# Kernel tuning notes

Hardware: AMD Instinct MI355X
Metric: run time of the kernel (lower is better)

The kernel has to match this reference:

```python
import jax, jax.numpy as jnp
import numpy as np

GRID_SIZE = 4
SPLINE_ORDER = 3
EDGE_DIM = 384


def make_grid():
    # efficient-KAN default grid_range [-1, 1]
    h = 2.0 / GRID_SIZE
    return (jnp.arange(-SPLINE_ORDER, GRID_SIZE + SPLINE_ORDER + 1, dtype=jnp.float32) * h - 1.0)


def b_splines(x, grid, k):
    # x: (N, d); grid: (G+2k+1,) shared across features -> (N, d, G+k)
    xe = x[..., None]
    bases = ((xe >= grid[:-1]) & (xe < grid[1:])).astype(x.dtype)
    for j in range(1, k + 1):
        bases = ((xe - grid[: -(j + 1)]) / (grid[j:-1] - grid[: -(j + 1)]) * bases[..., :-1]
                 + (grid[j + 1:] - xe) / (grid[j + 1:] - grid[1:-j]) * bases[..., 1:])
    return bases


def kan_linear(x, base_W, spline_W, grid):
    # efficient-KAN KANLinear: silu base path + spline path
    base = jax.nn.silu(x) @ base_W.T
    B = b_splines(x, grid, SPLINE_ORDER)          # (N, in, G+k)
    spline = jnp.einsum('nic,oic->no', B, spline_W)
    return base + spline


def gckan_layer(x, edge_index, edge_attr, p, grid):
    ea = edge_attr @ p['edge_W'].T + p['edge_b']          # (E, out)
    xt = x @ p['node_W'].T + p['node_b']                  # (N, out)
    row, col = edge_index[0], edge_index[1]
    msg = ea * xt[row]                                    # gather + multiply
    agg = jnp.zeros_like(xt).at[col].add(msg)             # scatter-add
    return kan_linear(agg, p['base_W'], p['spline_W'], grid)


def _layer_params(key, in_feat, out_feat):
    k1, k2, k3, k4 = jax.random.split(key, 4)
    coef = GRID_SIZE + SPLINE_ORDER
    return {
        'node_W': jax.random.normal(k1, (out_feat, in_feat), jnp.float32) / np.sqrt(in_feat),
        'node_b': jnp.zeros((out_feat,), jnp.float32),
        'edge_W': jax.random.normal(k2, (out_feat, EDGE_DIM), jnp.float32) / np.sqrt(EDGE_DIM),
        'edge_b': jnp.zeros((out_feat,), jnp.float32),
        'base_W': jax.random.normal(k3, (out_feat, out_feat), jnp.float32) / np.sqrt(out_feat),
        'spline_W': jax.random.normal(k4, (out_feat, out_feat, coef), jnp.float32) * (0.1 / np.sqrt(out_feat)),
    }


def setup_inputs() -> dict:
    N, E, F, H, C = 50000, 500000, 256, 256, 32
    key = jax.random.key(0)
    ks = jax.random.split(key, 6)
    inp = {
        'x': jax.random.normal(ks[0], (N, F), jnp.float32),
        'edge_index': jax.random.randint(ks[1], (2, E), 0, N, jnp.int32),
        'edge_attr': jax.random.normal(ks[2], (E, EDGE_DIM), jnp.float32),
    }
    p0 = _layer_params(ks[3], F, H)
    p1 = _layer_params(ks[4], H, H)
    po = _layer_params(ks[5], F + 2 * H, C)
    for tag, p in (('0', p0), ('1', p1), ('o', po)):
        for n, v in p.items():
            inp[n + tag] = v
    return inp


def reference(x, edge_index, edge_attr,
              node_W0, node_b0, edge_W0, edge_b0, base_W0, spline_W0,
              node_W1, node_b1, edge_W1, edge_b1, base_W1, spline_W1,
              node_Wo, node_bo, edge_Wo, edge_bo, base_Wo, spline_Wo):
    grid = make_grid()
    p0 = dict(node_W=node_W0, node_b=node_b0, edge_W=edge_W0, edge_b=edge_b0, base_W=base_W0, spline_W=spline_W0)
    p1 = dict(node_W=node_W1, node_b=node_b1, edge_W=edge_W1, edge_b=edge_b1, base_W=base_W1, spline_W=spline_W1)
    po = dict(node_W=node_Wo, node_b=node_bo, edge_W=edge_Wo, edge_b=edge_bo, base_W=base_Wo, spline_W=spline_Wo)
    skips = [x]
    h = gckan_layer(x, edge_index, edge_attr, p0, grid)
    skips.append(h)
    h = gckan_layer(h, edge_index, edge_attr, p1, grid)
    skips.append(h)
    h = jnp.concatenate(skips, axis=1)  # skip=True concat -> (N, F+2H)
    return gckan_layer(h, edge_index, edge_attr, po, grid)
```

## Files before the change

kernel.cpp:

```cpp
#include <hip/hip_runtime.h>


typedef __attribute__((ext_vector_type(4))) float f32x4;
typedef __attribute__((ext_vector_type(8))) short bf16x8;
typedef __attribute__((ext_vector_type(8))) unsigned short u16x8;
typedef __attribute__((ext_vector_type(4))) unsigned short u16x4;

__device__ __forceinline__ unsigned short f2bf(float f) {
    union { float f; unsigned u; } v; v.f = f;
    unsigned r = v.u + 0x7FFFu + ((v.u >> 16) & 1u);
    return (unsigned short)(r >> 16);
}

__device__ __forceinline__ float bf2f(unsigned short u) {
    union { unsigned u; float f; } v; v.u = ((unsigned)u) << 16;
    return v.f;
}

__device__ __forceinline__ float siluf(float x) {
    return x / (1.0f + __expf(-x));
}

__device__ __forceinline__ void gl16(const void* g, void* l) {
    __builtin_amdgcn_global_load_lds(
        (const __attribute__((address_space(1))) unsigned*)g,
        (__attribute__((address_space(3))) unsigned*)l, 16, 0, 0);
}

__device__ __forceinline__ void expand8(float x, float* o8) {
    float b[10];
#pragma unroll
    for (int i = 0; i < 10; ++i) {
        float ti = 0.5f * i - 2.5f;
        b[i] = (x >= ti && x < ti + 0.5f) ? 1.0f : 0.0f;
    }
#pragma unroll
    for (int j = 1; j <= 3; ++j) {
        float inv = 2.0f / (float)j;
#pragma unroll
        for (int i = 0; i < 10 - j; ++i) {
            float ti = 0.5f * i - 2.5f;
            float tj = 0.5f * (i + j + 1) - 2.5f;
            b[i] = (x - ti) * inv * b[i] + (tj - x) * inv * b[i + 1];
        }
    }
    o8[0] = siluf(x);
#pragma unroll
    for (int c = 0; c < 7; ++c) o8[c + 1] = b[c];
}

__global__ __launch_bounds__(256) void k_hist(
    const int* __restrict__ col, int* __restrict__ cnt, int E) {
    int i = blockIdx.x * 256 + threadIdx.x;
    if (i < E) atomicAdd(&cnt[col[i]], 1);
}

__global__ __launch_bounds__(1024) void k_scan(int* __restrict__ c, int N) {
    __shared__ int wsum[16];
    __shared__ int ctot;
    const int t = threadIdx.x;
    const int lane = t & 63, wid = t >> 6;
    int carry = 0;
    for (int base = 0; base < N; base += 1024) {
        int i = base + t;
        int v0 = (i < N) ? c[i] : 0;
        int v = v0;
#pragma unroll
        for (int off = 1; off < 64; off <<= 1) {
            int n = __shfl_up(v, (unsigned)off, 64);
            if (lane >= off) v += n;
        }
        if (lane == 63) wsum[wid] = v;
        __syncthreads();
        if (t < 16) {
            int s = wsum[t], sv = s;
#pragma unroll
            for (int off = 1; off < 16; off <<= 1) {
                int n = __shfl_up(sv, (unsigned)off, 16);
                if (t >= off) sv += n;
            }
            wsum[t] = sv - s;
            if (t == 15) ctot = sv;
        }
        __syncthreads();
        if (i < N) c[i] = carry + wsum[wid] + v - v0;
        carry += ctot;
        __syncthreads();
    }
}

__global__ __launch_bounds__(256) void k_scatter(
    const int* __restrict__ row, const int* __restrict__ col,
    int* __restrict__ cursor, int* __restrict__ rowS,
    int* __restrict__ colS, int* __restrict__ eidS, int E) {
    int i = blockIdx.x * 256 + threadIdx.x;
    if (i < E) {
        int c = col[i];
        int p = atomicAdd(&cursor[c], 1);
        rowS[p] = row[i];
        colS[p] = c;
        eidS[p] = i;
    }
}

__global__ __launch_bounds__(256) void pack_kt(
    const float* __restrict__ src, unsigned short* __restrict__ dst,
    int N, int K) {
    long idx = (long)blockIdx.x * 256 + threadIdx.x;
    if (idx >= (long)N * K) return;
    int n = (int)(idx / K), k = (int)(idx - (long)n * K);
    long o = (((long)(k >> 5) * 4 + ((k >> 3) & 3)) * N + n) * 8 + (k & 7);
    dst[o] = f2bf(src[idx]);
}

__global__ __launch_bounds__(256) void pack_kan_kt(
    const float* __restrict__ baseW, const float* __restrict__ splineW,
    unsigned short* __restrict__ dst, int N) {
    long idx = (long)blockIdx.x * 256 + threadIdx.x;
    if (idx >= (long)N * 2048) return;
    int n = (int)(idx >> 11), k = (int)(idx & 2047);
    int ic = k >> 3, c = k & 7;
    float v = (c == 0) ? baseW[(long)n * 256 + ic]
                       : splineW[((long)n * 256 + ic) * 7 + (c - 1)];
    long o = (((long)(k >> 5) * 4 + ((k >> 3) & 3)) * N + n) * 8 + (k & 7);
    dst[o] = f2bf(v);
}

template <bool TWO, bool WITH_O>
__global__ __launch_bounds__(256, 2) void ea_gemm7(
    const float* __restrict__ EA,
    const unsigned short* __restrict__ Wp0, const float* __restrict__ b0,
    const unsigned short* __restrict__ Wp1, const float* __restrict__ b1,
    const unsigned short* __restrict__ Wpo, const float* __restrict__ bo,
    unsigned short* __restrict__ O0, unsigned short* __restrict__ O1,
    unsigned short* __restrict__ Oo, int E) {
    constexpr int BSZ = TWO ? 32768 : 16384;
    constexpr int WOOFF = 8192 + 2 * BSZ;
    constexpr int SMEMSZ = WOOFF + (WITH_O ? 4096 : 0);
    __shared__ __align__(16) char smem[SMEMSZ];

    const int tid = threadIdx.x;
    const int wv = tid >> 6, lane = tid & 63;
    const int l15 = lane & 15, l4 = lane >> 4;
    const long m0 = (long)blockIdx.x * 64;

    f32x4 acc0[4][4] = {};
    f32x4 acc1[4][4] = {};
    f32x4 acco[4] = {};

    const int sr = tid >> 2, sg = tid & 3;
    const long arow = m0 + sr;
    const bool aok = arow < E;
    const float* aptr = EA + arow * 384 + sg * 8;
    const int awoff = sg * 1024 + ((sr ^ (sg << 2))) * 16;

    const char* wp0 = (const char*)Wp0;
    const char* wp1 = (const char*)Wp1;
    const char* wpo = (const char*)Wpo;
    const int ci = lane * 16;

#define ISSUE_B7(IT, BUF)                                                      \
    {                                                                          \
        _Pragma("unroll")                                                      \
        for (int g = 0; g < 4; ++g) {                                          \
            int ch = g * 4 + wv;                                               \
            gl16(wp0 + (long)(IT) * 16384 + ch * 1024 + ci,                    \
                 smem + 8192 + (BUF) * BSZ + ch * 1024);                       \
        }                                                                      \
        if (TWO) {                                                             \
            _Pragma("unroll")                                                  \
            for (int g = 0; g < 4; ++g) {                                      \
                int ch = g * 4 + wv;                                           \
                gl16(wp1 + (long)(IT) * 16384 + ch * 1024 + ci,                \
                     smem + 8192 + (BUF) * BSZ + 16384 + ch * 1024);           \
            }                                                                  \
        }                                                                      \
        __builtin_amdgcn_sched_barrier(0);                                     \
    }

#define ISSUE_WO7(IT, BUF)                                                     \
    {                                                                          \
        if (WITH_O && wv >= 2)                                                 \
            gl16(wpo + (long)(IT) * 2048 + (wv - 2) * 1024 + ci,               \
                 smem + WOOFF + (BUF) * 2048 + (wv - 2) * 1024);               \
        __builtin_amdgcn_sched_barrier(0);                                     \
    }

#define WRITE_A7(IT, VA, VB)                                                   \
    {                                                                          \
        u16x8 rr = {};                                                         \
        if (aok) {                                                             \
            rr[0] = f2bf((VA).x); rr[1] = f2bf((VA).y);                        \
            rr[2] = f2bf((VA).z); rr[3] = f2bf((VA).w);                        \
            rr[4] = f2bf((VB).x); rr[5] = f2bf((VB).y);                        \
            rr[6] = f2bf((VB).z); rr[7] = f2bf((VB).w);                        \
        }                                                                      \
        *(u16x8*)(smem + ((IT) & 1) * 4096 + awoff) = rr;                      \
        __builtin_amdgcn_sched_barrier(0);                                     \
    }

    const float4 z4 = make_float4(0.f, 0.f, 0.f, 0.f);
    {
        float4 s0 = z4, s1 = z4;
        if (aok) { s0 = *(const float4*)(aptr); s1 = *(const float4*)(aptr + 4); }
        WRITE_A7(0, s0, s1);
    }
    float4 r1a = z4, r1b = z4, r0a = z4, r0b = z4;
    if (aok) { r1a = *(const float4*)(aptr + 32); r1b = *(const float4*)(aptr + 36); }
    __builtin_amdgcn_sched_barrier(0);
    ISSUE_B7(0, 0);
    ISSUE_WO7(0, 0);
    if (aok) { r0a = *(const float4*)(aptr + 64); r0b = *(const float4*)(aptr + 68); }
    __builtin_amdgcn_sched_barrier(0);

#pragma unroll
    for (int it = 0; it < 12; ++it) {
        if (it <= 9) asm volatile("s_waitcnt vmcnt(2)" ::: "memory");
        else         asm volatile("s_waitcnt vmcnt(0)" ::: "memory");
        asm volatile("s_waitcnt lgkmcnt(0)" ::: "memory");
        __builtin_amdgcn_s_barrier();
        __builtin_amdgcn_sched_barrier(0);

        if (it < 11) {
            const int nbf = (it + 1) & 1;
            ISSUE_B7(it + 1, nbf);
            ISSUE_WO7(it + 1, nbf);
            if ((it + 1) & 1) { WRITE_A7(it + 1, r1a, r1b); }
            else              { WRITE_A7(it + 1, r0a, r0b); }
            if (it <= 8) {
                if ((it + 3) & 1) {
                    if (aok) {
                        r1a = *(const float4*)(aptr + (it + 3) * 32);
                        r1b = *(const float4*)(aptr + (it + 3) * 32 + 4);
                    }
                } else {
                    if (aok) {
                        r0a = *(const float4*)(aptr + (it + 3) * 32);
                        r0b = *(const float4*)(aptr + (it + 3) * 32 + 4);
                    }
                }
                __builtin_amdgcn_sched_barrier(0);
            }
        }

        const int buf = it & 1;
        bf16x8 af[4];
#pragma unroll
        for (int mi = 0; mi < 4; ++mi)
            af[mi] = *(const bf16x8*)(smem + buf * 4096 + l4 * 1024 +
                                      (((mi * 16 + l15) ^ (l4 << 2))) * 16);
        {
            bf16x8 bf0[4];
#pragma unroll
            for (int nj = 0; nj < 4; ++nj)
                bf0[nj] = *(const bf16x8*)(smem + 8192 + buf * BSZ + l4 * 4096 +
                                           (wv * 64 + nj * 16 + l15) * 16);
#pragma unroll
            for (int mi = 0; mi < 4; ++mi)
#pragma unroll
                for (int nj = 0; nj < 4; ++nj)
                    acc0[mi][nj] = __builtin_amdgcn_mfma_f32_16x16x32_bf16(
                        af[mi], bf0[nj], acc0[mi][nj], 0, 0, 0);
        }
        if (TWO) {
            bf16x8 bf1[4];
#pragma unroll
            for (int nj = 0; nj < 4; ++nj)
                bf1[nj] = *(const bf16x8*)(smem + 8192 + buf * BSZ + 16384 +
                                           l4 * 4096 + (wv * 64 + nj * 16 + l15) * 16);
#pragma unroll
            for (int mi = 0; mi < 4; ++mi)
#pragma unroll
                for (int nj = 0; nj < 4; ++nj)
                    acc1[mi][nj] = __builtin_amdgcn_mfma_f32_16x16x32_bf16(
                        af[mi], bf1[nj], acc1[mi][nj], 0, 0, 0);
        }
        if (WITH_O && wv < 2) {
            bf16x8 bov = *(const bf16x8*)(smem + WOOFF + buf * 2048 + l4 * 512 +
                                          (wv * 16 + l15) * 16);
#pragma unroll
            for (int mi = 0; mi < 4; ++mi)
                acco[mi] = __builtin_amdgcn_mfma_f32_16x16x32_bf16(
                    af[mi], bov, acco[mi], 0, 0, 0);
        }
    }
#undef ISSUE_B7
#undef ISSUE_WO7
#undef WRITE_A7

    const int nb2 = wv * 64;
    float bs0[4];
#pragma unroll
    for (int nj = 0; nj < 4; ++nj) bs0[nj] = b0[nb2 + nj * 16 + l15];
#pragma unroll
    for (int mi = 0; mi < 4; ++mi) {
#pragma unroll
        for (int r = 0; r < 4; ++r) {
            long e = m0 + mi * 16 + l4 * 4 + r;
            if (e < E) {
                unsigned short* dst = O0 + e * 256 + nb2 + l15;
#pragma unroll
                for (int nj = 0; nj < 4; ++nj)
                    dst[nj * 16] = f2bf(acc0[mi][nj][r] + bs0[nj]);
            }
        }
    }
    if (TWO) {
        float bs1[4];
#pragma unroll
        for (int nj = 0; nj < 4; ++nj) bs1[nj] = b1[nb2 + nj * 16 + l15];
#pragma unroll
        for (int mi = 0; mi < 4; ++mi) {
#pragma unroll
            for (int r = 0; r < 4; ++r) {
                long e = m0 + mi * 16 + l4 * 4 + r;
                if (e < E) {
                    unsigned short* dst = O1 + e * 256 + nb2 + l15;
#pragma unroll
                    for (int nj = 0; nj < 4; ++nj)
                        dst[nj * 16] = f2bf(acc1[mi][nj][r] + bs1[nj]);
                }
            }
        }
    }
    if (WITH_O && wv < 2) {
        float bso = bo[wv * 16 + l15];
#pragma unroll
        for (int mi = 0; mi < 4; ++mi) {
#pragma unroll
            for (int r = 0; r < 4; ++r) {
                long e = m0 + mi * 16 + l4 * 4 + r;
                if (e < E)
                    Oo[e * 32 + wv * 16 + l15] = f2bf(acco[mi][r] + bso);
            }
        }
    }
}

__global__ __launch_bounds__(256) void kan_mfma256_p(
    const float* __restrict__ AGG, const unsigned short* __restrict__ Wp,
    float* __restrict__ Y, int M) {
    __shared__ __align__(16) char smem[8192 + 2 * 16384];
    const int tid = threadIdx.x;
    const int wv = tid >> 6, lane = tid & 63;
    const int l15 = lane & 15, l4 = lane >> 4;
    const long m0 = (long)blockIdx.x * 64;
    f32x4 acc[4][4] = {};

    const int srow = tid & 63, sg = tid >> 6;
    const long arow = m0 + srow;
    const bool aok = arow < M;
    const float* aptr = AGG + arow * 256 + sg;
    const char* wp = (const char*)Wp;
    const int ci = lane * 16;
    const int awoff = sg * 1024 + srow * 16;

#define ISSUE_KB(IT, BUF)                                                      \
    {                                                                          \
        _Pragma("unroll")                                                      \
        for (int g = 0; g < 4; ++g) {                                          \
            int ch = g * 4 + wv;                                               \
            gl16(wp + (long)(IT) * 16384 + ch * 1024 + ci,                     \
                 smem + 8192 + (BUF) * 16384 + ch * 1024);                     \
        }                                                                      \
        __builtin_amdgcn_sched_barrier(0);                                     \
    }

    float xv0 = aok ? aptr[0] : 0.f;
    ISSUE_KB(0, 0);
    {
        float e8[8];
        expand8(xv0, e8);
        u16x8 ap;
#pragma unroll
        for (int c = 0; c < 8; ++c) ap[c] = f2bf(e8[c]);
        *(u16x8*)(smem + awoff) = ap;
    }
    float xv1 = aok ? aptr[4] : 0.f;
    __builtin_amdgcn_sched_barrier(0);

    for (int it = 0; it < 64; ++it) {
        if (it == 63) asm volatile("s_waitcnt vmcnt(0)" ::: "memory");
        else          asm volatile("s_waitcnt vmcnt(1)" ::: "memory");
        asm volatile("s_waitcnt lgkmcnt(0)" ::: "memory");
        __builtin_amdgcn_s_barrier();
        __builtin_amdgcn_sched_barrier(0);
        const int buf = it & 1, nbf = buf ^ 1;
        if (it < 63) {
            ISSUE_KB(it + 1, nbf);
            {
                float e8[8];
                expand8(xv1, e8);
                u16x8 ap;
#pragma unroll
                for (int c = 0; c < 8; ++c) ap[c] = f2bf(e8[c]);
                *(u16x8*)(smem + nbf * 4096 + awoff) = ap;
            }
            __builtin_amdgcn_sched_barrier(0);
            if (it < 62) {
                xv1 = aok ? aptr[(it + 2) * 4] : 0.f;
                __builtin_amdgcn_sched_barrier(0);
            }
        }
        bf16x8 af[4], bfv[4];
#pragma unroll
        for (int mi = 0; mi < 4; ++mi)
            af[mi] = *(const bf16x8*)(smem + buf * 4096 + l4 * 1024 +
                                      (mi * 16 + l15) * 16);
#pragma unroll
        for (int nj = 0; nj < 4; ++nj)
            bfv[nj] = *(const bf16x8*)(smem + 8192 + buf * 16384 + l4 * 4096 +
                                       (wv * 64 + nj * 16 + l15) * 16);
#pragma unroll
        for (int mi = 0; mi < 4; ++mi)
#pragma unroll
            for (int nj = 0; nj < 4; ++nj)
                acc[mi][nj] = __builtin_amdgcn_mfma_f32_16x16x32_bf16(
                    af[mi], bfv[nj], acc[mi][nj], 0, 0, 0);
    }
#undef ISSUE_KB

    const int nb = wv * 64;
#pragma unroll
    for (int mi = 0; mi < 4; ++mi) {
#pragma unroll
        for (int r = 0; r < 4; ++r) {
            long gm = m0 + mi * 16 + l4 * 4 + r;
            if (gm < M) {
#pragma unroll
                for (int nj = 0; nj < 4; ++nj)
                    Y[gm * 256 + nb + nj * 16 + l15] = acc[mi][nj][r];
            }
        }
    }
}

template <int K>
__global__ __launch_bounds__(256) void node_mfma_p(
    const float* __restrict__ X, const unsigned short* __restrict__ Wp,
    const float* __restrict__ bias, unsigned short* __restrict__ Y, int M) {
    __shared__ __align__(16) char smem[8192 + 2 * 16384];
    const int tid = threadIdx.x;
    const int wv = tid >> 6, lane = tid & 63;
    const int l15 = lane & 15, l4 = lane >> 4;
    const long m0 = (long)blockIdx.x * 64;
    f32x4 acc[4][4] = {};
    constexpr int NIT = K / 32;

    const int sr = tid >> 2, sg = tid & 3;
    const long arow = m0 + sr;
    const bool aok = arow < M;
    const float* aptr = X + arow * K + sg * 8;
    const int awoff = sg * 1024 + ((sr ^ (sg << 2))) * 16;
    const char* wp = (const char*)Wp;
    const int ci = lane * 16;

#define ISSUE_NB(IT, BUF)                                                      \
    {                                                                          \
        _Pragma("unroll")                                                      \
        for (int g = 0; g < 4; ++g) {                                          \
            int ch = g * 4 + wv;                                               \
            gl16(wp + (long)(IT) * 16384 + ch * 1024 + ci,                     \
                 smem + 8192 + (BUF) * 16384 + ch * 1024);                     \
        }                                                                      \
        __builtin_amdgcn_sched_barrier(0);                                     \
    }

#define WRITE_NA(BUF)                                                          \
    {                                                                          \
        u16x8 rr = {};                                                         \
        if (aok) {                                                             \
            rr[0] = f2bf(a0v.x); rr[1] = f2bf(a0v.y);                          \
            rr[2] = f2bf(a0v.z); rr[3] = f2bf(a0v.w);                          \
            rr[4] = f2bf(a1v.x); rr[5] = f2bf(a1v.y);                          \
            rr[6] = f2bf(a1v.z); rr[7] = f2bf(a1v.w);                          \
        }                                                                      \
        *(u16x8*)(smem + (BUF) * 4096 + awoff) = rr;                           \
        __builtin_amdgcn_sched_barrier(0);                                     \
    }

    ISSUE_NB(0, 0);
    float4 a0v = make_float4(0.f, 0.f, 0.f, 0.f);
    float4 a1v = make_float4(0.f, 0.f, 0.f, 0.f);
    if (aok) { a0v = *(const float4*)(aptr); a1v = *(const float4*)(aptr + 4); }
    WRITE_NA(0);
    if (aok) { a0v = *(const float4*)(aptr + 32); a1v = *(const float4*)(aptr + 36); }
    __builtin_amdgcn_sched_barrier(0);

#pragma unroll
    for (int it = 0; it < NIT; ++it) {
        if (it == NIT - 1) asm volatile("s_waitcnt vmcnt(0)" ::: "memory");
        else               asm volatile("s_waitcnt vmcnt(2)" ::: "memory");
        asm volatile("s_waitcnt lgkmcnt(0)" ::: "memory");
        __builtin_amdgcn_s_barrier();
        __builtin_amdgcn_sched_barrier(0);
        const int buf = it & 1, nbf = buf ^ 1;
        if (it < NIT - 1) {
            ISSUE_NB(it + 1, nbf);
            WRITE_NA(nbf);
            if (it < NIT - 2) {
                if (aok) {
                    a0v = *(const float4*)(aptr + (it + 2) * 32);
                    a1v = *(const float4*)(aptr + (it + 2) * 32 + 4);
                }
                __builtin_amdgcn_sched_barrier(0);
            }
        }
        bf16x8 af[4], bfv[4];
#pragma unroll
        for (int mi = 0; mi < 4; ++mi)
            af[mi] = *(const bf16x8*)(smem + buf * 4096 + l4 * 1024 +
                                      (((mi * 16 + l15) ^ (l4 << 2))) * 16);
#pragma unroll
        for (int nj = 0; nj < 4; ++nj)
            bfv[nj] = *(const bf16x8*)(smem + 8192 + buf * 16384 + l4 * 4096 +
                                       (wv * 64 + nj * 16 + l15) * 16);
#pragma unroll
        for (int mi = 0; mi < 4; ++mi)
#pragma unroll
            for (int nj = 0; nj < 4; ++nj)
                acc[mi][nj] = __builtin_amdgcn_mfma_f32_16x16x32_bf16(
                    af[mi], bfv[nj], acc[mi][nj], 0, 0, 0);
    }
#undef ISSUE_NB
#undef WRITE_NA

    const int nb = wv * 64;
    float bs[4];
#pragma unroll
    for (int nj = 0; nj < 4; ++nj) bs[nj] = bias[nb + nj * 16 + l15];
#pragma unroll
    for (int mi = 0; mi < 4; ++mi) {
#pragma unroll
        for (int r = 0; r < 4; ++r) {
            long gm = m0 + mi * 16 + l4 * 4 + r;
            if (gm < M) {
#pragma unroll
                for (int nj = 0; nj < 4; ++nj)
                    Y[gm * 256 + nb + nj * 16 + l15] = f2bf(acc[mi][nj][r] + bs[nj]);
            }
        }
    }
}

__global__ __launch_bounds__(256) void msg256(
    const unsigned short* __restrict__ EAr, const unsigned short* __restrict__ XT,
    const int* __restrict__ rowS, const int* __restrict__ colS,
    const int* __restrict__ eidS, float* __restrict__ AGG, int E) {
    __shared__ __align__(16) unsigned short eas[64][264];
    __shared__ int rows_s[64];
    __shared__ int cols_s[64];
    const int tid = threadIdx.x;
    const long m0 = (long)blockIdx.x * 64;

    const int r = tid >> 2, s = tid & 3;
    {
        long p = m0 + r;
        if (p < E) {
            const unsigned short* src = EAr + (long)eidS[p] * 256 + s * 8;
#pragma unroll
            for (int k = 0; k < 8; ++k)
                *(u16x8*)&eas[r][s * 8 + k * 32] = *(const u16x8*)(src + k * 32);
        } else {
            u16x8 z = {};
#pragma unroll
            for (int k = 0; k < 8; ++k) *(u16x8*)&eas[r][s * 8 + k * 32] = z;
        }
    }
    if (tid < 64) {
        long p = m0 + tid;
        cols_s[tid] = (p < E) ? colS[p] : -1;
        rows_s[tid] = (p < E) ? rowS[p] : 0;
    }
    __syncthreads();

    const int c = tid;
    float sum = 0.f;
    int cur = cols_s[0];
    int runstart = 0;
#pragma unroll 1
    for (int g = 0; g < 8; ++g) {
        float xv[8];
#pragma unroll
        for (int j = 0; j < 8; ++j)
            xv[j] = bf2f(XT[(long)rows_s[g * 8 + j] * 256 + c]);
#pragma unroll
        for (int j = 0; j < 8; ++j) {
            int e = g * 8 + j;
            int cc = cols_s[e];
            if (cc != cur) {
                if (cur >= 0) {
                    float* dst = AGG + (long)cur * 256 + c;
                    if (runstart > 0) *dst = sum;
                    else atomicAdd(dst, sum);
                }
                cur = cc; runstart = e; sum = 0.f;
            }
            sum += bf2f(eas[e][c]) * xv[j];
        }
    }
    if (cur >= 0) {
        atomicAdd(AGG + (long)cur * 256 + c, sum);
    }
}

__global__ __launch_bounds__(256) void msg32(
    const unsigned short* __restrict__ EAro, const unsigned short* __restrict__ XT,
    const int* __restrict__ rowS, const int* __restrict__ colS,
    const int* __restrict__ eidS, float* __restrict__ AGG, int E) {
    __shared__ __align__(16) unsigned short eas[256][36];
    __shared__ int rows_s[256];
    __shared__ int cols_s[256];
    __shared__ int eid_s[256];
    const int tid = threadIdx.x;
    const long m0 = (long)blockIdx.x * 256;

    {
        long p = m0 + tid;
        cols_s[tid] = (p < E) ? colS[p] : -1;
        rows_s[tid] = (p < E) ? rowS[p] : 0;
        eid_s[tid]  = (p < E) ? eidS[p] : -1;
    }
    __syncthreads();
    const int rr0 = tid >> 2, s = tid & 3;
#pragma unroll
    for (int ps = 0; ps < 4; ++ps) {
        int rr = ps * 64 + rr0;
        int eid = eid_s[rr];
        u16x8 v = {};
        if (eid >= 0) v = *(const u16x8*)(EAro + (long)eid * 32 + s * 8);
        *(u16x8*)&eas[rr][s * 8] = v;
    }
    __syncthreads();

    const int c = tid & 31, sb = tid >> 5;
    const int e0 = sb * 32;
    float sum = 0.f;
    int cur = cols_s[e0];
    int runstart = e0;
#pragma unroll 1
    for (int g = 0; g < 4; ++g) {
        float xv[8];
#pragma unroll
        for (int j = 0; j < 8; ++j)
            xv[j] = bf2f(XT[(long)rows_s[e0 + g * 8 + j] * 32 + c]);
#pragma unroll
        for (int j = 0; j < 8; ++j) {
            int e = e0 + g * 8 + j;
            int cc = cols_s[e];
            if (cc != cur) {
                if (cur >= 0) {
                    float* dst = AGG + (long)cur * 32 + c;
                    if (runstart > 0 && cols_s[runstart - 1] != cur) *dst = sum;
                    else atomicAdd(dst, sum);
                }
                cur = cc; runstart = e; sum = 0.f;
            }
            sum += bf2f(eas[e][c]) * xv[j];
        }
    }
    if (cur >= 0) {
        int eend = e0 + 32;
        float* dst = AGG + (long)cur * 32 + c;
        bool oks = (runstart > 0 && cols_s[runstart - 1] != cur);
        bool oke = (eend < 256 && cols_s[eend] != cur);
        if (oks && oke) *dst = sum;
        else atomicAdd(dst, sum);
    }
}

__global__ __launch_bounds__(256) void node_cat_mfma(
    const float* __restrict__ X, const float* __restrict__ H0,
    const float* __restrict__ H1, const unsigned short* __restrict__ Wh,
    const float* __restrict__ bias, unsigned short* __restrict__ Y, int M) {
    __shared__ __align__(16) unsigned short As[4][256][8];
    __shared__ __align__(16) unsigned short Bs[4][32][8];
    const int tid = threadIdx.x;
    const int wv = tid >> 6, lane = tid & 63;
    const int l15 = lane & 15, l4 = lane >> 4;
    const long m0 = (long)blockIdx.x * 256;
    f32x4 acc[4][2] = {};

    const int sr = tid >> 3;
    const int sq = (tid & 7) * 4;
    const int sg2 = sq >> 3, so2 = sq & 7;

    for (int it = 0; it < 24; ++it) {
        const int k0 = it * 32;
        const float* src = (it < 8) ? X : (it < 16) ? H0 : H1;
        const int kk = k0 & 255;
        float4 va[8];
#pragma unroll
        for (int j = 0; j < 8; ++j) {
            long r_ = m0 + j * 32 + sr;
            va[j] = (r_ < M) ? *(const float4*)(src + r_ * 256 + kk + sq)
                             : make_float4(0.f, 0.f, 0.f, 0.f);
        }
        u16x8 bv = {};
        if (tid < 128)
            bv = *(const u16x8*)(Wh + (long)(tid >> 2) * 768 + k0 + (tid & 3) * 8);
        __syncthreads();
#pragma unroll
        for (int j = 0; j < 8; ++j) {
            u16x4 ap;
            ap[0] = f2bf(va[j].x); ap[1] = f2bf(va[j].y);
            ap[2] = f2bf(va[j].z); ap[3] = f2bf(va[j].w);
            *(u16x4*)&As[sg2][j * 32 + sr][so2] = ap;
        }
        if (tid < 128) *(u16x8*)&Bs[tid & 3][tid >> 2][0] = bv;
        __syncthreads();
        bf16x8 af[4], bfv[2];
#pragma unroll
        for (int mi = 0; mi < 4; ++mi)
            af[mi] = *(const bf16x8*)&As[l4][wv * 64 + mi * 16 + l15][0];
#pragma unroll
        for (int nj = 0; nj < 2; ++nj)
            bfv[nj] = *(const bf16x8*)&Bs[l4][nj * 16 + l15][0];
#pragma unroll
        for (int mi = 0; mi < 4; ++mi)
#pragma unroll
            for (int nj = 0; nj < 2; ++nj)
                acc[mi][nj] = __builtin_amdgcn_mfma_f32_16x16x32_bf16(
                    af[mi], bfv[nj], acc[mi][nj], 0, 0, 0);
    }

#pragma unroll
    for (int mi = 0; mi < 4; ++mi) {
#pragma unroll
        for (int r = 0; r < 4; ++r) {
            long gm = m0 + wv * 64 + mi * 16 + l4 * 4 + r;
            if (gm < M) {
#pragma unroll
                for (int nj = 0; nj < 2; ++nj) {
                    int o = nj * 16 + l15;
                    Y[gm * 32 + o] = f2bf(acc[mi][nj][r] + bias[o]);
                }
            }
        }
    }
}

__global__ __launch_bounds__(256) void kan_gemm32(
    const float* __restrict__ AGG, const float* __restrict__ Wc,
    float* __restrict__ Y, int M) {
    __shared__ float As[64][36];
    __shared__ float Bs[32][36];
    const int tid = threadIdx.x;
    const int tx = tid & 15, ty = tid >> 4;
    const int m0 = blockIdx.x * 64;
    float acc[4][2] = {{0.f, 0.f}, {0.f, 0.f}, {0.f, 0.f}, {0.f, 0.f}};
    const int er = tid >> 2, ef = tid & 3;
    const int em = m0 + er;
    for (int ic = 0; ic < 32; ic += 4) {
        float xv = (em < M) ? AGG[(long)em * 32 + ic + ef] : 0.f;
        float e8[8];
        expand8(xv, e8);
        *(float4*)&As[er][ef * 8] = make_float4(e8[0], e8[1], e8[2], e8[3]);
        *(float4*)&As[er][ef * 8 + 4] = make_float4(e8[4], e8[5], e8[6], e8[7]);
        {
            int o = tid >> 3, k4 = (tid & 7) * 4;
            *(float4*)&Bs[o][k4] = *(const float4*)&Wc[(long)o * 256 + ic * 8 + k4];
        }
        __syncthreads();
#pragma unroll
        for (int kk = 0; kk < 32; ++kk) {
            float a_[4], b_[2];
#pragma unroll
            for (int i = 0; i < 4; ++i) a_[i] = As[ty * 4 + i][kk];
#pragma unroll
            for (int j = 0; j < 2; ++j) b_[j] = Bs[tx * 2 + j][kk];
#pragma unroll
            for (int i = 0; i < 4; ++i)
#pragma unroll
                for (int j = 0; j < 2; ++j) acc[i][j] = fmaf(a_[i], b_[j], acc[i][j]);
        }
        __syncthreads();
    }
#pragma unroll
    for (int i = 0; i < 4; ++i) {
        int gm = m0 + ty * 4 + i;
        if (gm >= M) continue;
#pragma unroll
        for (int j = 0; j < 2; ++j) Y[(long)gm * 32 + tx * 2 + j] = acc[i][j];
    }
}

__global__ __launch_bounds__(256) void cvt_bf16(
    const float* __restrict__ s, unsigned short* __restrict__ d, int n) {
    int i = blockIdx.x * 256 + threadIdx.x;
    if (i < n) d[i] = f2bf(s[i]);
}

__global__ __launch_bounds__(256) void pack_kan_f32(
    const float* __restrict__ baseW, const float* __restrict__ splineW,
    float* __restrict__ Wc, int n) {
    int idx = blockIdx.x * 256 + threadIdx.x;
    if (idx >= n) return;
    float* dst = Wc + (long)idx * 8;
    dst[0] = baseW[idx];
    const float* sw = splineW + (long)idx * 7;
#pragma unroll
    for (int c = 0; c < 7; ++c) dst[1 + c] = sw[c];
}

extern "C" void kernel_launch(void* const* d_in, const int* in_sizes, int n_in,
                              void* d_out, int out_size, void* d_ws, size_t ws_size,
                              hipStream_t stream) {
    const float* x          = (const float*)d_in[0];
    const int*   edge_index = (const int*)d_in[1];
    const float* edge_attr  = (const float*)d_in[2];
    const float* node_W0 = (const float*)d_in[3];
    const float* node_b0 = (const float*)d_in[4];
    const float* edge_W0 = (const float*)d_in[5];
    const float* edge_b0 = (const float*)d_in[6];
    const float* base_W0 = (const float*)d_in[7];
    const float* spline_W0 = (const float*)d_in[8];
    const float* node_W1 = (const float*)d_in[9];
    const float* node_b1 = (const float*)d_in[10];
    const float* edge_W1 = (const float*)d_in[11];
    const float* edge_b1 = (const float*)d_in[12];
    const float* base_W1 = (const float*)d_in[13];
    const float* spline_W1 = (const float*)d_in[14];
    const float* node_Wo = (const float*)d_in[15];
    const float* node_bo = (const float*)d_in[16];
    const float* edge_Wo = (const float*)d_in[17];
    const float* edge_bo = (const float*)d_in[18];
    const float* base_Wo = (const float*)d_in[19];
    const float* spline_Wo = (const float*)d_in[20];
    float* out = (float*)d_out;

    const int N = in_sizes[0] / 256;
    const int E = in_sizes[1] / 2;

    float* ws  = (float*)d_ws;
    unsigned short* xt = (unsigned short*)ws;
    float* agg = ws + (long)N * 256;
    float* h0  = agg + (long)N * 256;
    float* h1  = h0 + (long)N * 256;
    float* Wco = h1 + (long)N * 256;
    unsigned short* Wp0  = (unsigned short*)(Wco + 32 * 256);
    unsigned short* Wp1  = Wp0 + 98304;
    unsigned short* Wpo  = Wp1 + 98304;
    unsigned short* nWp0 = Wpo + 12288;
    unsigned short* nWp1 = nWp0 + 65536;
    unsigned short* Wc0p = nWp1 + 65536;
    unsigned short* Wc1p = Wc0p + 524288;
    unsigned short* nWoh = Wc1p + 524288;
    int* cursor = (int*)(nWoh + 24576);
    int* rowS   = cursor + (N + 1);
    int* colS   = rowS + E;
    int* eidS   = colS + E;
    unsigned short* EAr0 = (unsigned short*)(((uintptr_t)(eidS + E) + 255) & ~(uintptr_t)255);
    const int nt256 = (E + 255) / 256;
    const long Epad = (long)nt256 * 256;
    unsigned short* EAr1 = EAr0 + Epad * 256;

    const size_t need2 = (size_t)((char*)(EAr1 + Epad * 256 + Epad * 32) - (char*)d_ws);
    const bool two = ws_size >= need2;
    unsigned short* EAro = two ? (EAr1 + Epad * 256) : (EAr0 + Epad * 256);

    const int* row = edge_index;
    const int* col = edge_index + E;

    const int nb64 = (N + 63) / 64;
    const int eb64 = (E + 63) / 64;
    const int eb256 = (E + 255) / 256;
    const int nb256 = (N + 255) / 256;

    hipMemsetAsync(cursor, 0, (size_t)(N + 1) * sizeof(int), stream);
    k_hist<<<eb256, 256, 0, stream>>>(col, cursor, E);
    k_scan<<<1, 1024, 0, stream>>>(cursor, N);
    k_scatter<<<eb256, 256, 0, stream>>>(row, col, cursor, rowS, colS, eidS, E);

    pack_kt<<<(256 * 384 + 255) / 256, 256, 0, stream>>>(edge_W0, Wp0, 256, 384);
    pack_kt<<<(256 * 384 + 255) / 256, 256, 0, stream>>>(edge_W1, Wp1, 256, 384);
    pack_kt<<<(32 * 384 + 255) / 256, 256, 0, stream>>>(edge_Wo, Wpo, 32, 384);
    pack_kt<<<(256 * 256 + 255) / 256, 256, 0, stream>>>(node_W0, nWp0, 256, 256);
    pack_kt<<<(256 * 256 + 255) / 256, 256, 0, stream>>>(node_W1, nWp1, 256, 256);
    pack_kan_kt<<<(256 * 2048 + 255) / 256, 256, 0, stream>>>(base_W0, spline_W0, Wc0p, 256);
    pack_kan_kt<<<(256 * 2048 + 255) / 256, 256, 0, stream>>>(base_W1, spline_W1, Wc1p, 256);
    cvt_bf16<<<(32 * 768 + 255) / 256, 256, 0, stream>>>(node_Wo, nWoh, 32 * 768);
    pack_kan_f32<<<(32 * 32 + 255) / 256, 256, 0, stream>>>(base_Wo, spline_Wo, Wco, 32 * 32);

    if (two) {
        ea_gemm7<true, true><<<eb64, 256, 0, stream>>>(
            edge_attr, Wp0, edge_b0, Wp1, edge_b1, Wpo, edge_bo,
            EAr0, EAr1, EAro, E);
    } else {
        ea_gemm7<false, true><<<eb64, 256, 0, stream>>>(
            edge_attr, Wp0, edge_b0, Wp0, edge_b0, Wpo, edge_bo,
            EAr0, EAr0, EAro, E);
    }

    hipMemsetAsync(agg, 0, (size_t)N * 256 * sizeof(float), stream);
    node_mfma_p<256><<<nb64, 256, 0, stream>>>(x, nWp0, node_b0, xt, N);
    msg256<<<eb64, 256, 0, stream>>>(EAr0, xt, rowS, colS, eidS, agg, E);
    kan_mfma256_p<<<nb64, 256, 0, stream>>>(agg, Wc0p, h0, N);

    if (!two) {
        ea_gemm7<false, false><<<eb64, 256, 0, stream>>>(
            edge_attr, Wp1, edge_b1, Wp1, edge_b1, Wpo, edge_bo,
            EAr0, EAr0, EAro, E);
    }
    hipMemsetAsync(agg, 0, (size_t)N * 256 * sizeof(float), stream);
    node_mfma_p<256><<<nb64, 256, 0, stream>>>(h0, nWp1, node_b1, xt, N);
    msg256<<<eb64, 256, 0, stream>>>(two ? EAr1 : EAr0, xt, rowS, colS, eidS, agg, E);
    kan_mfma256_p<<<nb64, 256, 0, stream>>>(agg, Wc1p, h1, N);

    hipMemsetAsync(agg, 0, (size_t)N * 32 * sizeof(float), stream);
    node_cat_mfma<<<nb256, 256, 0, stream>>>(x, h0, h1, nWoh, node_bo, xt, N);
    msg32<<<eb256, 256, 0, stream>>>(EAro, xt, rowS, colS, eidS, agg, E);
    kan_gemm32<<<nb64, 256, 0, stream>>>(agg, Wco, out, N);
}
```

Before: 1.319 ms.

## Load GEMM weight fragments directly from global memory instead of staging through LDS

The edge-attribute GEMM, node GEMM and KAN GEMM kernels stop staging the packed bf16 weight tiles into double-buffered LDS with global_load_lds. Each wave now reads its B fragments straight from global memory (served mostly from cache, since every block shares the same weights). This shrinks LDS use to the A buffers only and adds a min-blocks hint of 2 to node and KAN kernels, aiming for more occupancy and fewer barrier and waitcnt stalls. The trade-off is that global-load latency now sits directly before the MFMAs with no explicit prefetch, so throughput relies on L1/L2 hits and on occupancy to hide that latency.

Result: no change. 1.328 ms (+0.7%).

```diff
diff --git a/kernel.cpp b/kernel.cpp
--- a/kernel.cpp
+++ b/kernel.cpp
@@ -19,12 +19,6 @@
 
 __device__ __forceinline__ float siluf(float x) {
     return x / (1.0f + __expf(-x));
-}
-
-__device__ __forceinline__ void gl16(const void* g, void* l) {
-    __builtin_amdgcn_global_load_lds(
-        (const __attribute__((address_space(1))) unsigned*)g,
-        (__attribute__((address_space(3))) unsigned*)l, 16, 0, 0);
 }
 
 __device__ __forceinline__ void expand8(float x, float* o8) {
@@ -127,17 +121,14 @@
 }
 
 template <bool TWO, bool WITH_O>
-__global__ __launch_bounds__(256, 2) void ea_gemm7(
+__global__ __launch_bounds__(256, 2) void ea_gemm8(
     const float* __restrict__ EA,
     const unsigned short* __restrict__ Wp0, const float* __restrict__ b0,
     const unsigned short* __restrict__ Wp1, const float* __restrict__ b1,
     const unsigned short* __restrict__ Wpo, const float* __restrict__ bo,
     unsigned short* __restrict__ O0, unsigned short* __restrict__ O1,
     unsigned short* __restrict__ Oo, int E) {
-    constexpr int BSZ = TWO ? 32768 : 16384;
-    constexpr int WOOFF = 8192 + 2 * BSZ;
-    constexpr int SMEMSZ = WOOFF + (WITH_O ? 4096 : 0);
-    __shared__ __align__(16) char smem[SMEMSZ];
+    __shared__ __align__(16) char smem[8192];
 
     const int tid = threadIdx.x;
     const int wv = tid >> 6, lane = tid & 63;
@@ -154,39 +145,11 @@
     const float* aptr = EA + arow * 384 + sg * 8;
     const int awoff = sg * 1024 + ((sr ^ (sg << 2))) * 16;
 
-    const char* wp0 = (const char*)Wp0;
-    const char* wp1 = (const char*)Wp1;
-    const char* wpo = (const char*)Wpo;
-    const int ci = lane * 16;
-
-#define ISSUE_B7(IT, BUF)                                                      \
-    {                                                                          \
-        _Pragma("unroll")                                                      \
-        for (int g = 0; g < 4; ++g) {                                          \
-            int ch = g * 4 + wv;                                               \
-            gl16(wp0 + (long)(IT) * 16384 + ch * 1024 + ci,                    \
-                 smem + 8192 + (BUF) * BSZ + ch * 1024);                       \
-        }                                                                      \
-        if (TWO) {                                                             \
-            _Pragma("unroll")                                                  \
-            for (int g = 0; g < 4; ++g) {                                      \
-                int ch = g * 4 + wv;                                           \
-                gl16(wp1 + (long)(IT) * 16384 + ch * 1024 + ci,                \
-                     smem + 8192 + (BUF) * BSZ + 16384 + ch * 1024);           \
-            }                                                                  \
-        }                                                                      \
-        __builtin_amdgcn_sched_barrier(0);                                     \
-    }
-
-#define ISSUE_WO7(IT, BUF)                                                     \
-    {                                                                          \
-        if (WITH_O && wv >= 2)                                                 \
-            gl16(wpo + (long)(IT) * 2048 + (wv - 2) * 1024 + ci,               \
-                 smem + WOOFF + (BUF) * 2048 + (wv - 2) * 1024);               \
-        __builtin_amdgcn_sched_barrier(0);                                     \
-    }
-
-#define WRITE_A7(IT, VA, VB)                                                   \
+    const char* bp0 = (const char*)Wp0 + l4 * 4096 + wv * 1024 + l15 * 16;
+    const char* bp1 = (const char*)Wp1 + l4 * 4096 + wv * 1024 + l15 * 16;
+    const char* bpo = (const char*)Wpo + l4 * 512 + (wv * 16 + l15) * 16;
+
+#define WRITE_A8(IT, VA, VB)                                                   \
     {                                                                          \
         u16x8 rr = {};                                                         \
         if (aok) {                                                             \
@@ -196,37 +159,29 @@
             rr[6] = f2bf((VB).z); rr[7] = f2bf((VB).w);                        \
         }                                                                      \
         *(u16x8*)(smem + ((IT) & 1) * 4096 + awoff) = rr;                      \
-        __builtin_amdgcn_sched_barrier(0);                                     \
     }
 
     const float4 z4 = make_float4(0.f, 0.f, 0.f, 0.f);
     {
         float4 s0 = z4, s1 = z4;
         if (aok) { s0 = *(const float4*)(aptr); s1 = *(const float4*)(aptr + 4); }
-        WRITE_A7(0, s0, s1);
+        WRITE_A8(0, s0, s1);
     }
     float4 r1a = z4, r1b = z4, r0a = z4, r0b = z4;
-    if (aok) { r1a = *(const float4*)(aptr + 32); r1b = *(const float4*)(aptr + 36); }
-    __builtin_amdgcn_sched_barrier(0);
-    ISSUE_B7(0, 0);
-    ISSUE_WO7(0, 0);
-    if (aok) { r0a = *(const float4*)(aptr + 64); r0b = *(const float4*)(aptr + 68); }
-    __builtin_amdgcn_sched_barrier(0);
+    if (aok) {
+        r1a = *(const float4*)(aptr + 32); r1b = *(const float4*)(aptr + 36);
+        r0a = *(const float4*)(aptr + 64); r0b = *(const float4*)(aptr + 68);
+    }
 
 #pragma unroll
     for (int it = 0; it < 12; ++it) {
-        if (it <= 9) asm volatile("s_waitcnt vmcnt(2)" ::: "memory");
-        else         asm volatile("s_waitcnt vmcnt(0)" ::: "memory");
         asm volatile("s_waitcnt lgkmcnt(0)" ::: "memory");
         __builtin_amdgcn_s_barrier();
         __builtin_amdgcn_sched_barrier(0);
 
         if (it < 11) {
-            const int nbf = (it + 1) & 1;
-            ISSUE_B7(it + 1, nbf);
-            ISSUE_WO7(it + 1, nbf);
-            if ((it + 1) & 1) { WRITE_A7(it + 1, r1a, r1b); }
-            else              { WRITE_A7(it + 1, r0a, r0b); }
+            if ((it + 1) & 1) { WRITE_A8(it + 1, r1a, r1b); }
+            else              { WRITE_A8(it + 1, r0a, r0b); }
             if (it <= 8) {
                 if ((it + 3) & 1) {
                     if (aok) {
@@ -239,7 +194,6 @@
                         r0b = *(const float4*)(aptr + (it + 3) * 32 + 4);
                     }
                 }
-                __builtin_amdgcn_sched_barrier(0);
             }
         }
 
@@ -253,8 +207,7 @@
             bf16x8 bf0[4];
 #pragma unroll
             for (int nj = 0; nj < 4; ++nj)
-                bf0[nj] = *(const bf16x8*)(smem + 8192 + buf * BSZ + l4 * 4096 +
-                                           (wv * 64 + nj * 16 + l15) * 16);
+                bf0[nj] = *(const bf16x8*)(bp0 + (long)it * 16384 + nj * 256);
 #pragma unroll
             for (int mi = 0; mi < 4; ++mi)
 #pragma unroll
@@ -266,8 +219,7 @@
             bf16x8 bf1[4];
 #pragma unroll
             for (int nj = 0; nj < 4; ++nj)
-                bf1[nj] = *(const bf16x8*)(smem + 8192 + buf * BSZ + 16384 +
-                                           l4 * 4096 + (wv * 64 + nj * 16 + l15) * 16);
+                bf1[nj] = *(const bf16x8*)(bp1 + (long)it * 16384 + nj * 256);
 #pragma unroll
             for (int mi = 0; mi < 4; ++mi)
 #pragma unroll
@@ -276,17 +228,14 @@
                         af[mi], bf1[nj], acc1[mi][nj], 0, 0, 0);
         }
         if (WITH_O && wv < 2) {
-            bf16x8 bov = *(const bf16x8*)(smem + WOOFF + buf * 2048 + l4 * 512 +
-                                          (wv * 16 + l15) * 16);
+            bf16x8 bov = *(const bf16x8*)(bpo + (long)it * 2048);
 #pragma unroll
             for (int mi = 0; mi < 4; ++mi)
                 acco[mi] = __builtin_amdgcn_mfma_f32_16x16x32_bf16(
                     af[mi], bov, acco[mi], 0, 0, 0);
         }
     }
-#undef ISSUE_B7
-#undef ISSUE_WO7
-#undef WRITE_A7
+#undef WRITE_A8
 
     const int nb2 = wv * 64;
     float bs0[4];
@@ -337,10 +286,10 @@
     }
 }
 
-__global__ __launch_bounds__(256) void kan_mfma256_p(
+__global__ __launch_bounds__(256, 2) void kan_mfma256_r(
     const float* __restrict__ AGG, const unsigned short* __restrict__ Wp,
     float* __restrict__ Y, int M) {
-    __shared__ __align__(16) char smem[8192 + 2 * 16384];
+    __shared__ __align__(16) char smem[8192];
     const int tid = threadIdx.x;
     const int wv = tid >> 6, lane = tid & 63;
     const int l15 = lane & 15, l4 = lane >> 4;
@@ -351,24 +300,11 @@
     const long arow = m0 + srow;
     const bool aok = arow < M;
     const float* aptr = AGG + arow * 256 + sg;
-    const char* wp = (const char*)Wp;
-    const int ci = lane * 16;
     const int awoff = sg * 1024 + srow * 16;
-
-#define ISSUE_KB(IT, BUF)                                                      \
-    {                                                                          \
-        _Pragma("unroll")                                                      \
-        for (int g = 0; g < 4; ++g) {                                          \
-            int ch = g * 4 + wv;                                               \
-            gl16(wp + (long)(IT) * 16384 + ch * 1024 + ci,                     \
-                 smem + 8192 + (BUF) * 16384 + ch * 1024);                     \
-        }                                                                      \
-        __builtin_amdgcn_sched_barrier(0);                                     \
-    }
-
-    float xv0 = aok ? aptr[0] : 0.f;
-    ISSUE_KB(0, 0);
+    const char* bp = (const char*)Wp + l4 * 4096 + wv * 1024 + l15 * 16;
+
     {
+        float xv0 = aok ? aptr[0] : 0.f;
         float e8[8];
         expand8(xv0, e8);
         u16x8 ap;
@@ -377,30 +313,20 @@
         *(u16x8*)(smem + awoff) = ap;
     }
     float xv1 = aok ? aptr[4] : 0.f;
-    __builtin_amdgcn_sched_barrier(0);
 
     for (int it = 0; it < 64; ++it) {
-        if (it == 63) asm volatile("s_waitcnt vmcnt(0)" ::: "memory");
-        else          asm volatile("s_waitcnt vmcnt(1)" ::: "memory");
         asm volatile("s_waitcnt lgkmcnt(0)" ::: "memory");
         __builtin_amdgcn_s_barrier();
         __builtin_amdgcn_sched_barrier(0);
-        const int buf = it & 1, nbf = buf ^ 1;
+        const int buf = it & 1;
         if (it < 63) {
-            ISSUE_KB(it + 1, nbf);
-            {
-                float e8[8];
-                expand8(xv1, e8);
-                u16x8 ap;
-#pragma unroll
-                for (int c = 0; c < 8; ++c) ap[c] = f2bf(e8[c]);
-                *(u16x8*)(smem + nbf * 4096 + awoff) = ap;
-            }
-            __builtin_amdgcn_sched_barrier(0);
-            if (it < 62) {
-                xv1 = aok ? aptr[(it + 2) * 4] : 0.f;
-                __builtin_amdgcn_sched_barrier(0);
-            }
+            float e8[8];
+            expand8(xv1, e8);
+            u16x8 ap;
+#pragma unroll
+            for (int c = 0; c < 8; ++c) ap[c] = f2bf(e8[c]);
+            *(u16x8*)(smem + (buf ^ 1) * 4096 + awoff) = ap;
+            if (it < 62) xv1 = aok ? aptr[(it + 2) * 4] : 0.f;
         }
         bf16x8 af[4], bfv[4];
 #pragma unroll
@@ -409,8 +335,7 @@
                                       (mi * 16 + l15) * 16);
 #pragma unroll
         for (int nj = 0; nj < 4; ++nj)
-            bfv[nj] = *(const bf16x8*)(smem + 8192 + buf * 16384 + l4 * 4096 +
-                                       (wv * 64 + nj * 16 + l15) * 16);
+            bfv[nj] = *(const bf16x8*)(bp + (long)it * 16384 + nj * 256);
 #pragma unroll
         for (int mi = 0; mi < 4; ++mi)
 #pragma unroll
@@ -418,7 +343,6 @@
                 acc[mi][nj] = __builtin_amdgcn_mfma_f32_16x16x32_bf16(
                     af[mi], bfv[nj], acc[mi][nj], 0, 0, 0);
     }
-#undef ISSUE_KB
 
     const int nb = wv * 64;
 #pragma unroll
@@ -436,10 +360,10 @@
 }
 
 template <int K>
-__global__ __launch_bounds__(256) void node_mfma_p(
+__global__ __launch_bounds__(256, 2) void node_mfma_r(
     const float* __restrict__ X, const unsigned short* __restrict__ Wp,
     const float* __restrict__ bias, unsigned short* __restrict__ Y, int M) {
-    __shared__ __align__(16) char smem[8192 + 2 * 16384];
+    __shared__ __align__(16) char smem[8192];
     const int tid = threadIdx.x;
     const int wv = tid >> 6, lane = tid & 63;
     const int l15 = lane & 15, l4 = lane >> 4;
@@ -452,60 +376,55 @@
     const bool aok = arow < M;
     const float* aptr = X + arow * K + sg * 8;
     const int awoff = sg * 1024 + ((sr ^ (sg << 2))) * 16;
-    const char* wp = (const char*)Wp;
-    const int ci = lane * 16;
-
-#define ISSUE_NB(IT, BUF)                                                      \
-    {                                                                          \
-        _Pragma("unroll")                                                      \
-        for (int g = 0; g < 4; ++g) {                                          \
-            int ch = g * 4 + wv;                                               \
-            gl16(wp + (long)(IT) * 16384 + ch * 1024 + ci,                     \
-                 smem + 8192 + (BUF) * 16384 + ch * 1024);                     \
-        }                                                                      \
-        __builtin_amdgcn_sched_barrier(0);                                     \
-    }
-
-#define WRITE_NA(BUF)                                                          \
+    const char* bp = (const char*)Wp + l4 * 4096 + wv * 1024 + l15 * 16;
+
+#define WRITE_NA8(IT, VA, VB)                                                  \
     {                                                                          \
         u16x8 rr = {};                                                         \
         if (aok) {                                                             \
-            rr[0] = f2bf(a0v.x); rr[1] = f2bf(a0v.y);                          \
-            rr[2] = f2bf(a0v.z); rr[3] = f2bf(a0v.w);                          \
-            rr[4] = f2bf(a1v.x); rr[5] = f2bf(a1v.y);                          \
-            rr[6] = f2bf(a1v.z); rr[7] = f2bf(a1v.w);                          \
+            rr[0] = f2bf((VA).x); rr[1] = f2bf((VA).y);                        \
+            rr[2] = f2bf((VA).z); rr[3] = f2bf((VA).w);                        \
+            rr[4] = f2bf((VB).x); rr[5] = f2bf((VB).y);                        \
+            rr[6] = f2bf((VB).z); rr[7] = f2bf((VB).w);                        \
         }                                                                      \
-        *(u16x8*)(smem + (BUF) * 4096 + awoff) = rr;                           \
-        __builtin_amdgcn_sched_barrier(0);                                     \
-    }
-
-    ISSUE_NB(0, 0);
-    float4 a0v = make_float4(0.f, 0.f, 0.f, 0.f);
-    float4 a1v = make_float4(0.f, 0.f, 0.f, 0.f);
-    if (aok) { a0v = *(const float4*)(aptr); a1v = *(const float4*)(aptr + 4); }
-    WRITE_NA(0);
-    if (aok) { a0v = *(const float4*)(aptr + 32); a1v = *(const float4*)(aptr + 36); }
-    __builtin_amdgcn_sched_barrier(0);
+        *(u16x8*)(smem + ((IT) & 1) * 4096 + awoff) = rr;                      \
+    }
+
+    const float4 z4 = make_float4(0.f, 0.f, 0.f, 0.f);
+    {
+        float4 s0 = z4, s1 = z4;
+        if (aok) { s0 = *(const float4*)(aptr); s1 = *(const float4*)(aptr + 4); }
+        WRITE_NA8(0, s0, s1);
+    }
+    float4 r1a = z4, r1b = z4, r0a = z4, r0b = z4;
+    if (aok) {
+        r1a = *(const float4*)(aptr + 32); r1b = *(const float4*)(aptr + 36);
+        r0a = *(const float4*)(aptr + 64); r0b = *(const float4*)(aptr + 68);
+    }
 
 #pragma unroll
     for (int it = 0; it < NIT; ++it) {
-        if (it == NIT - 1) asm volatile("s_waitcnt vmcnt(0)" ::: "memory");
-        else               asm volatile("s_waitcnt vmcnt(2)" ::: "memory");
         asm volatile("s_waitcnt lgkmcnt(0)" ::: "memory");
         __builtin_amdgcn_s_barrier();
         __builtin_amdgcn_sched_barrier(0);
-        const int buf = it & 1, nbf = buf ^ 1;
         if (it < NIT - 1) {
-            ISSUE_NB(it + 1, nbf);
-            WRITE_NA(nbf);
-            if (it < NIT - 2) {
-                if (aok) {
-                    a0v = *(const float4*)(aptr + (it + 2) * 32);
-                    a1v = *(const float4*)(aptr + (it + 2) * 32 + 4);
+            if ((it + 1) & 1) { WRITE_NA8(it + 1, r1a, r1b); }
+            else              { WRITE_NA8(it + 1, r0a, r0b); }
+            if (it <= NIT - 4) {
+                if ((it + 3) & 1) {
+                    if (aok) {
+                        r1a = *(const float4*)(aptr + (it + 3) * 32);
+                        r1b = *(const float4*)(aptr + (it + 3) * 32 + 4);
+                    }
+                } else {
+                    if (aok) {
+                        r0a = *(const float4*)(aptr + (it + 3) * 32);
+                        r0b = *(const float4*)(aptr + (it + 3) * 32 + 4);
+                    }
                 }
-                __builtin_amdgcn_sched_barrier(0);
-            }
-        }
+            }
+        }
+        const int buf = it & 1;
         bf16x8 af[4], bfv[4];
 #pragma unroll
         for (int mi = 0; mi < 4; ++mi)
@@ -513,8 +432,7 @@
                                       (((mi * 16 + l15) ^ (l4 << 2))) * 16);
 #pragma unroll
         for (int nj = 0; nj < 4; ++nj)
-            bfv[nj] = *(const bf16x8*)(smem + 8192 + buf * 16384 + l4 * 4096 +
-                                       (wv * 64 + nj * 16 + l15) * 16);
+            bfv[nj] = *(const bf16x8*)(bp + (long)it * 16384 + nj * 256);
 #pragma unroll
         for (int mi = 0; mi < 4; ++mi)
 #pragma unroll
@@ -522,8 +440,7 @@
                 acc[mi][nj] = __builtin_amdgcn_mfma_f32_16x16x32_bf16(
                     af[mi], bfv[nj], acc[mi][nj], 0, 0, 0);
     }
-#undef ISSUE_NB
-#undef WRITE_NA
+#undef WRITE_NA8
 
     const int nb = wv * 64;
     float bs[4];
@@ -883,29 +800,29 @@
     pack_kan_f32<<<(32 * 32 + 255) / 256, 256, 0, stream>>>(base_Wo, spline_Wo, Wco, 32 * 32);
 
     if (two) {
-        ea_gemm7<true, true><<<eb64, 256, 0, stream>>>(
+        ea_gemm8<true, true><<<eb64, 256, 0, stream>>>(
             edge_attr, Wp0, edge_b0, Wp1, edge_b1, Wpo, edge_bo,
             EAr0, EAr1, EAro, E);
     } else {
-        ea_gemm7<false, true><<<eb64, 256, 0, stream>>>(
+        ea_gemm8<false, true><<<eb64, 256, 0, stream>>>(
             edge_attr, Wp0, edge_b0, Wp0, edge_b0, Wpo, edge_bo,
             EAr0, EAr0, EAro, E);
     }
 
     hipMemsetAsync(agg, 0, (size_t)N * 256 * sizeof(float), stream);
-    node_mfma_p<256><<<nb64, 256, 0, stream>>>(x, nWp0, node_b0, xt, N);
+    node_mfma_r<256><<<nb64, 256, 0, stream>>>(x, nWp0, node_b0, xt, N);
     msg256<<<eb64, 256, 0, stream>>>(EAr0, xt, rowS, colS, eidS, agg, E);
-    kan_mfma256_p<<<nb64, 256, 0, stream>>>(agg, Wc0p, h0, N);
+    kan_mfma256_r<<<nb64, 256, 0, stream>>>(agg, Wc0p, h0, N);
 
     if (!two) {
-        ea_gemm7<false, false><<<eb64, 256, 0, stream>>>(
+        ea_gemm8<false, false><<<eb64, 256, 0, stream>>>(
             edge_attr, Wp1, edge_b1, Wp1, edge_b1, Wpo, edge_bo,
             EAr0, EAr0, EAro, E);
     }
     hipMemsetAsync(agg, 0, (size_t)N * 256 * sizeof(float), stream);
-    node_mfma_p<256><<<nb64, 256, 0, stream>>>(h0, nWp1, node_b1, xt, N);
+    node_mfma_r<256><<<nb64, 256, 0, stream>>>(h0, nWp1, node_b1, xt, N);
     msg256<<<eb64, 256, 0, stream>>>(two ? EAr1 : EAr0, xt, rowS, colS, eidS, agg, E);
-    kan_mfma256_p<<<nb64, 256, 0, stream>>>(agg, Wc1p, h1, N);
+    kan_mfma256_r<<<nb64, 256, 0, stream>>>(agg, Wc1p, h1, N);
 
     hipMemsetAsync(agg, 0, (size_t)N * 32 * sizeof(float), stream);
     node_cat_mfma<<<nb256, 256, 0, stream>>>(x, h0, h1, nWoh, node_bo, xt, N);
```
